# Kernel tuning notes

Hardware: AMD Instinct MI355X
Metric: run time of the kernel (lower is better)

The kernel has to match this reference:

```python
import math
import jax, jax.numpy as jnp
import numpy as np

B, N, C = 64, 1024, 128
RATIO = 0.5
EDGE_P = 0.02  # sparsity of the random binary adjacency


def setup_inputs() -> dict:
    key = jax.random.key(0)
    kx, ka, kw = jax.random.split(key, 3)
    x = jax.random.normal(kx, (B, N, C), dtype=jnp.float32)
    # binary adjacency (realistic graph input); module symmetrizes + clips anyway
    adj = (jax.random.uniform(ka, (B, N, N)) < EDGE_P).astype(jnp.float32)
    # TopKPooling learnable score weight (PyG initializes uniform; normal is fine for a baseline)
    w = jax.random.normal(kw, (C,), dtype=jnp.float32)
    return {"x": x, "adj": adj, "w": w}


def reference(x, adj, w):
    # x: [B, N, C], adj: [B, N, N], w: [C]
    b, n, c = x.shape
    k = int(math.ceil(RATIO * n))  # same k for every graph -> fully batched

    # per-sample: adj_tmp = adj + adj.T; adj_tmp[adj_tmp > 1] = 1
    a = adj + jnp.swapaxes(adj, 1, 2)
    a = jnp.minimum(a, 1.0)

    # TopKPooling score: tanh((x . w) / ||w||), select top-k nodes per graph
    score = jnp.tanh(jnp.einsum("bnc,c->bn", x, w) / jnp.linalg.norm(w))
    top_scores, perm = jax.lax.top_k(score, k)          # [B, k] each, descending

    # gated node features: x[perm] * score[perm]
    x_pool = jnp.take_along_axis(x, perm[..., None], axis=1) * top_scores[..., None]  # [B,k,C]

    # pooled dense adjacency: edges among selected nodes (to_dense_adj counts edges,
    # so entries are 1 where a nonzero edge existed) + 1 on diagonal from add_self_loops
    a_rows = jnp.take_along_axis(a, perm[:, :, None], axis=1)        # [B, k, N]
    a_sub = jnp.take_along_axis(a_rows, perm[:, None, :], axis=2)    # [B, k, k]
    adj_pooled = (a_sub != 0).astype(x.dtype) + jnp.eye(k, dtype=x.dtype)[None]

    return x_pool, adj_pooled
```

## Files before the change

### kernel.cpp

```cpp
#include <hip/hip_runtime.h>
#include <math.h>

#define NB 64
#define NN 1024
#define NC 128
#define NK 512

__global__ __launch_bounds__(1024) void scorerank_kernel(
    const float* __restrict__ x, const float* __restrict__ w,
    int* __restrict__ perm, float* __restrict__ gate, int* __restrict__ inv,
    float* __restrict__ x_pool)
{
    __shared__ __align__(16) double s[NN];
    __shared__ int rp[1024];
    __shared__ double s_rnw;
    __shared__ int sel_nr[256];
    __shared__ float sel_g[256];
    __shared__ int scount;
    const int i = blockIdx.x;
    const int b = (i & 7) + ((i >> 5) << 3);
    const int q = (i >> 3) & 3;
    const int t = threadIdx.x;

    const int c0 = (t & 15) * 8;
    const float4 wa = *(const float4*)(w + c0);
    const float4 wb = *(const float4*)(w + c0 + 4);
    #pragma unroll 4
    for (int pass = 0; pass < 16; ++pass) {
        int row = pass * 64 + (t >> 4);
        const float* xr = x + ((size_t)b * NN + row) * NC + c0;
        float4 a  = *(const float4*)xr;
        float4 bb = *(const float4*)(xr + 4);
        double acc = (double)a.x * wa.x + (double)a.y * wa.y
                   + (double)a.z * wa.z + (double)a.w * wa.w
                   + (double)bb.x * wb.x + (double)bb.y * wb.y
                   + (double)bb.z * wb.z + (double)bb.w * wb.w;
        acc += __shfl_xor(acc, 1, 64);
        acc += __shfl_xor(acc, 2, 64);
        acc += __shfl_xor(acc, 4, 64);
        acc += __shfl_xor(acc, 8, 64);
        if ((t & 15) == 0) s[row] = acc;
    }
    if (t < 64) {
        double p = (double)w[t] * (double)w[t]
                 + (double)w[t + 64] * (double)w[t + 64];
        #pragma unroll
        for (int off = 32; off > 0; off >>= 1)
            p += __shfl_xor(p, off, 64);
        if (t == 0) s_rnw = 1.0 / sqrt(p);
    }
    if (t == 0) scount = 0;
    __syncthreads();

    const int n  = q * 256 + (t & 255);
    const int jc = t >> 8;
    const double my = s[n];
    int r = 0;
    #pragma unroll 8
    for (int j = jc * 256; j < jc * 256 + 256; j += 2) {
        double2 o = *(const double2*)&s[j];
        r += (o.x > my) || ((o.x == my) && (j < n));
        r += (o.y > my) || ((o.y == my) && (j + 1 < n));
    }
    rp[t] = r;
    __syncthreads();
    if (jc == 0) {
        int rr = rp[t] + rp[t + 256] + rp[t + 512] + rp[t + 768];
        inv[b * NN + n] = (rr < NK) ? rr : -1;
        if (rr < NK) {
            float gv = (float)tanh(my * s_rnw);
            perm[b * NK + rr] = n;
            gate[b * NK + rr] = gv;
            int slot = atomicAdd(&scount, 1);
            sel_nr[slot] = (n << 16) | rr;
            sel_g[slot]  = gv;
        }
    }
    __syncthreads();

    const int cnt = scount;
    const int rowSlot = t >> 5;
    const int lane = t & 31;
    for (int base = 0; base < cnt; base += 32) {
        int idx = base + rowSlot;
        if (idx < cnt) {
            int nr = sel_nr[idx];
            int n2 = nr >> 16, rr = nr & 0xffff;
            float g = sel_g[idx];
            float4 v = *(const float4*)(x + ((size_t)b * NN + n2) * NC + lane * 4);
            v.x *= g; v.y *= g; v.z *= g; v.w *= g;
            *(float4*)(x_pool + ((size_t)b * NK + rr) * NC + lane * 4) = v;
        }
    }
}

__global__ __launch_bounds__(1024) void adj_scan_kernel(
    const float* __restrict__ adj, const int* __restrict__ perm,
    const int* __restrict__ inv, unsigned* __restrict__ bm)
{
    __shared__ unsigned bits[64 * 17];
    __shared__ int sinv[NN];
    const int b = blockIdx.x >> 3;
    const int chunk = blockIdx.x & 7;
    const int t = threadIdx.x;
    for (int idx = t; idx < 64 * 17; idx += 1024) bits[idx] = 0;
    for (int idx = t; idx < NN; idx += 1024) sinv[idx] = inv[b * NN + idx];
    __syncthreads();

    const float* ab = adj + (size_t)b * NN * NN;
    const int* permb = perm + b * NK + chunk * 64;
    const int g  = t >> 8;
    const int lt = t & 255;

    int il = g;
    float4 v0 = *(const float4*)(ab + (size_t)permb[il] * NN + lt * 4);
    float4 v1 = *(const float4*)(ab + (size_t)permb[il + 4] * NN + lt * 4);
    float4 v2 = *(const float4*)(ab + (size_t)permb[il + 8] * NN + lt * 4);
    float4 v3 = *(const float4*)(ab + (size_t)permb[il + 12] * NN + lt * 4);
    for (int it = 0; it < 16; ++it) {
        float4 vn = v0;
        if (it < 12)
            vn = *(const float4*)(ab + (size_t)permb[il + 16] * NN + lt * 4);
        #pragma unroll
        for (int u = 0; u < 4; ++u) {
            if (((const float*)&v0)[u] != 0.0f) {
                int j = sinv[lt * 4 + u];
                if (j >= 0)
                    atomicOr(&bits[il * 17 + (j >> 5)], 1u << (j & 31));
            }
        }
        v0 = v1; v1 = v2; v2 = v3; v3 = vn; il += 4;
    }
    __syncthreads();
    {
        int dil = t & 63, w = t >> 6;
        bm[(size_t)b * 8192 + w * 512 + chunk * 64 + dil] = bits[dil * 17 + w];
    }
}

__global__ __launch_bounds__(1024) void adj_write_kernel(
    const unsigned* __restrict__ bm, float* __restrict__ out)
{
    __shared__ unsigned tcb[2 * 512];
    __shared__ unsigned fws[64 * 17];
    const int b = blockIdx.x >> 3;
    const int slab = blockIdx.x & 7;
    const int t = threadIdx.x;
    const unsigned* bmb = bm + (size_t)b * 8192;
    {
        int e = t >> 9, j = t & 511;
        tcb[t] = bmb[(slab * 2 + e) * 512 + j];
    }
    {
        int il = t & 63, wi = t >> 6;
        fws[il * 17 + wi] = bmb[wi * 512 + slab * 64 + il];
    }
    __syncthreads();

    float* ob = out + ((size_t)b * NK + slab * 64) * NK;
    #pragma unroll
    for (int it = 0; it < 8; ++it) {
        int lid = it * 1024 + t;
        int i_loc = lid >> 7;
        int i = slab * 64 + i_loc;
        int j4 = (lid & 127) * 4;
        unsigned fw = fws[i_loc * 17 + (j4 >> 5)];
        uint4 tq = *(const uint4*)&tcb[(i_loc >> 5) * 512 + j4];
        float4 res;
        float* rpn = (float*)&res;
        const unsigned* tp = (const unsigned*)&tq;
        #pragma unroll
        for (int e = 0; e < 4; ++e) {
            unsigned bit = ((fw >> ((j4 + e) & 31)) | (tp[e] >> (i & 31))) & 1u;
            float f = (float)bit;
            if (i == j4 + e) f += 1.0f;
            rpn[e] = f;
        }
        *(float4*)(ob + (size_t)i_loc * NK + j4) = res;
    }
}

extern "C" void kernel_launch(void* const* d_in, const int* in_sizes, int n_in,
                              void* d_out, int out_size, void* d_ws, size_t ws_size,
                              hipStream_t stream) {
    const float* x   = (const float*)d_in[0];
    const float* adj = (const float*)d_in[1];
    const float* w   = (const float*)d_in[2];
    float* out = (float*)d_out;

    char* p = (char*)d_ws;
    unsigned* bm   = (unsigned*)p;  p += sizeof(unsigned) * NB * 16 * NK;
    int*      perm = (int*)p;       p += sizeof(int) * NB * NK;
    float*    gate = (float*)p;     p += sizeof(float) * NB * NK;
    int*      inv  = (int*)p;

    float* x_pool     = out;
    float* adj_pooled = out + (size_t)NB * NK * NC;

    scorerank_kernel<<<NB * 4, 1024, 0, stream>>>(x, w, perm, gate, inv, x_pool);
    adj_scan_kernel<<<NB * 8, 1024, 0, stream>>>(adj, perm, inv, bm);
    adj_write_kernel<<<NB * 8, 1024, 0, stream>>>(bm, adj_pooled);
}
```

Baseline: 66.26 us.

## Split score and rank kernels, rank via packed integer keys

The fused score+rank kernel is split in two. The first computes per-node dot-product scores once into a workspace buffer, so the x read is no longer repeated four times per graph. The second ranks 128 nodes per block over 8 blocks per graph. It encodes each double score as a monotone 64-bit integer with the node index packed into the low 10 bits, turning the tie-broken comparison into a single unsigned compare. This adds a kernel launch and a global round-trip for scores. Overwriting the low mantissa bits can merge near-equal scores and change the ordering slightly.

```diff
diff --git a/kernel.cpp b/kernel.cpp
--- a/kernel.cpp
+++ b/kernel.cpp
@@ -6,28 +6,19 @@
 #define NC 128
 #define NK 512
 
-__global__ __launch_bounds__(1024) void scorerank_kernel(
+__global__ __launch_bounds__(1024) void score_kernel(
     const float* __restrict__ x, const float* __restrict__ w,
-    int* __restrict__ perm, float* __restrict__ gate, int* __restrict__ inv,
-    float* __restrict__ x_pool)
-{
-    __shared__ __align__(16) double s[NN];
-    __shared__ int rp[1024];
-    __shared__ double s_rnw;
-    __shared__ int sel_nr[256];
-    __shared__ float sel_g[256];
-    __shared__ int scount;
+    double* __restrict__ sacc)
+{
     const int i = blockIdx.x;
-    const int b = (i & 7) + ((i >> 5) << 3);
-    const int q = (i >> 3) & 3;
-    const int t = threadIdx.x;
-
+    const int b = i >> 2, q = i & 3;
+    const int t = threadIdx.x;
     const int c0 = (t & 15) * 8;
     const float4 wa = *(const float4*)(w + c0);
     const float4 wb = *(const float4*)(w + c0 + 4);
-    #pragma unroll 4
-    for (int pass = 0; pass < 16; ++pass) {
-        int row = pass * 64 + (t >> 4);
+    #pragma unroll
+    for (int pass = 0; pass < 4; ++pass) {
+        int row = q * 256 + pass * 64 + (t >> 4);
         const float* xr = x + ((size_t)b * NN + row) * NC + c0;
         float4 a  = *(const float4*)xr;
         float4 bb = *(const float4*)(xr + 4);
@@ -39,7 +30,33 @@
         acc += __shfl_xor(acc, 2, 64);
         acc += __shfl_xor(acc, 4, 64);
         acc += __shfl_xor(acc, 8, 64);
-        if ((t & 15) == 0) s[row] = acc;
+        if ((t & 15) == 0) sacc[(size_t)b * NN + row] = acc;
+    }
+}
+
+__global__ __launch_bounds__(1024) void rank_xpool_kernel(
+    const double* __restrict__ sacc, const float* __restrict__ x,
+    const float* __restrict__ w, int* __restrict__ perm,
+    float* __restrict__ gate, int* __restrict__ inv,
+    float* __restrict__ x_pool)
+{
+    __shared__ __align__(16) unsigned long long keys[NN];
+    __shared__ int rp[1024];
+    __shared__ double s_rnw;
+    __shared__ int sel_nr[128];
+    __shared__ float sel_g[128];
+    __shared__ int scount;
+    const int i = blockIdx.x;
+    const int b = (i & 7) + ((i >> 6) << 3);
+    const int h = (i >> 3) & 7;
+    const int t = threadIdx.x;
+
+    {
+        double sv = sacc[(size_t)b * NN + t];
+        long long bits = __double_as_longlong(sv);
+        unsigned long long mono =
+            (unsigned long long)(bits ^ ((bits >> 63) | 0x8000000000000000LL));
+        keys[t] = (mono & ~1023ULL) | (unsigned long long)(1023 - t);
     }
     if (t < 64) {
         double p = (double)w[t] * (double)w[t]
@@ -52,27 +69,31 @@
     if (t == 0) scount = 0;
     __syncthreads();
 
-    const int n  = q * 256 + (t & 255);
-    const int jc = t >> 8;
-    const double my = s[n];
+    const int n  = h * 128 + (t & 127);
+    const int jc = t >> 7;
+    const unsigned long long mykey = keys[n];
     int r = 0;
     #pragma unroll 8
-    for (int j = jc * 256; j < jc * 256 + 256; j += 2) {
-        double2 o = *(const double2*)&s[j];
-        r += (o.x > my) || ((o.x == my) && (j < n));
-        r += (o.y > my) || ((o.y == my) && (j + 1 < n));
+    for (int j2 = 0; j2 < 64; ++j2) {
+        ulonglong2 kk = *(const ulonglong2*)&keys[jc * 128 + j2 * 2];
+        r += (kk.x > mykey);
+        r += (kk.y > mykey);
     }
     rp[t] = r;
     __syncthreads();
-    if (jc == 0) {
-        int rr = rp[t] + rp[t + 256] + rp[t + 512] + rp[t + 768];
-        inv[b * NN + n] = (rr < NK) ? rr : -1;
+    if (t < 128) {
+        int rr = 0;
+        #pragma unroll
+        for (int c = 0; c < 8; ++c) rr += rp[c * 128 + t];
+        int n2 = h * 128 + t;
+        inv[b * NN + n2] = (rr < NK) ? rr : -1;
         if (rr < NK) {
-            float gv = (float)tanh(my * s_rnw);
-            perm[b * NK + rr] = n;
+            double sv = sacc[(size_t)b * NN + n2];
+            float gv = (float)tanh(sv * s_rnw);
+            perm[b * NK + rr] = n2;
             gate[b * NK + rr] = gv;
             int slot = atomicAdd(&scount, 1);
-            sel_nr[slot] = (n << 16) | rr;
+            sel_nr[slot] = (n2 << 16) | rr;
             sel_g[slot]  = gv;
         }
     }
@@ -189,6 +210,7 @@
     float* out = (float*)d_out;
 
     char* p = (char*)d_ws;
+    double*   sacc = (double*)p;    p += sizeof(double) * NB * NN;
     unsigned* bm   = (unsigned*)p;  p += sizeof(unsigned) * NB * 16 * NK;
     int*      perm = (int*)p;       p += sizeof(int) * NB * NK;
     float*    gate = (float*)p;     p += sizeof(float) * NB * NK;
@@ -197,7 +219,8 @@
     float* x_pool     = out;
     float* adj_pooled = out + (size_t)NB * NK * NC;
 
-    scorerank_kernel<<<NB * 4, 1024, 0, stream>>>(x, w, perm, gate, inv, x_pool);
+    score_kernel<<<NB * 4, 1024, 0, stream>>>(x, w, sacc);
+    rank_xpool_kernel<<<NB * 8, 1024, 0, stream>>>(sacc, x, w, perm, gate, inv, x_pool);
     adj_scan_kernel<<<NB * 8, 1024, 0, stream>>>(adj, perm, inv, bm);
     adj_write_kernel<<<NB * 8, 1024, 0, stream>>>(bm, adj_pooled);
 }
```

New measurement: 56.18 us. 1.18x faster.
